# Kernel tuning notes

Measured on AMD Instinct MI355X. Metric: run time of the kernel, lower is better.

## Reference

```python
import jax, jax.numpy as jnp
import numpy as np

B, N, C = 8, 4096, 768
H = 12
D = C // H  # 64


def setup_inputs() -> dict:
    key = jax.random.key(0)
    k1, k2, k3 = jax.random.split(key, 3)
    x = jax.random.normal(k1, (B, N, C), dtype=jnp.float32)
    Wqkv = jax.random.normal(k2, (C, 3 * C), dtype=jnp.float32) * (C ** -0.5)
    Wproj = jax.random.normal(k3, (C, C), dtype=jnp.float32) * (C ** -0.5)
    bproj = jnp.zeros((C,), dtype=jnp.float32)
    return {"x": x, "Wqkv": Wqkv, "Wproj": Wproj, "bproj": bproj}


def reference(x, Wqkv, Wproj, bproj):
    b, n, c = x.shape
    qkv = x @ Wqkv  # [B,N,3C]
    qkv = qkv.reshape(b, n, 3, H, D).transpose(2, 0, 3, 1, 4)  # [3,B,H,N,D]
    q, k, v = qkv[0], qkv[1], qkv[2]
    # softmax over the sequence axis (dim=-2 in torch => N)
    k = jax.nn.softmax(k, axis=-2)
    # context: [B,H,D,D] -- small d x d intermediate
    context = jnp.einsum('bhnd,bhne->bhde', k, v)
    out = jnp.einsum('bhnd,bhde->bhne', q, context)  # [B,H,N,D]
    out = out.transpose(0, 2, 1, 3).reshape(b, n, c)  # b h n d -> b n (h d)
    return out @ Wproj + bproj
```

## Files before the change

kernel.cpp:

```cpp
#include <hip/hip_runtime.h>
#include <cstdint>
#include <cstddef>


typedef __bf16 bf8_t __attribute__((ext_vector_type(8)));
typedef float f4_t __attribute__((ext_vector_type(4)));

#define DEV_INLINE __device__ __forceinline__

DEV_INLINE void gload16(const void* g, void* l) {
  __builtin_amdgcn_global_load_lds(
      (const __attribute__((address_space(1))) void*)g,
      (__attribute__((address_space(3))) void*)l, 16, 0, 0);
}

__global__ __launch_bounds__(256) void cast_f32_bf16(const float* __restrict__ in,
                                                     __bf16* __restrict__ out, int n4) {
  int i = blockIdx.x * 256 + threadIdx.x;
  if (i >= n4) return;
  float4 f = ((const float4*)in)[i];
  union { __bf16 h[4]; uint2 u; } o;
  o.h[0] = (__bf16)f.x; o.h[1] = (__bf16)f.y; o.h[2] = (__bf16)f.z; o.h[3] = (__bf16)f.w;
  ((uint2*)out)[i] = o.u;
}

__global__ __launch_bounds__(256) void transpose_cast(const float* __restrict__ in,
                                                      __bf16* __restrict__ out, int R, int C) {
  __shared__ float t[64][65];
  const int tilesR = R >> 6;
  const int tr = blockIdx.x % tilesR, tc = blockIdx.x / tilesR;
  const int tx = threadIdx.x & 63, ty = threadIdx.x >> 6;
  const int r0 = tr * 64, c0 = tc * 64;
#pragma unroll
  for (int p = 0; p < 16; p++) {
    int r = p * 4 + ty;
    t[r][tx] = in[(size_t)(r0 + r) * C + c0 + tx];
  }
  __syncthreads();
#pragma unroll
  for (int p = 0; p < 16; p++) {
    int c = p * 4 + ty;
    out[(size_t)(c0 + c) * R + r0 + tx] = (__bf16)t[tx][c];
  }
}

__global__ __launch_bounds__(256) void wq_cast(const float* __restrict__ in,
                                               __bf16* __restrict__ out) {
  int o = blockIdx.x * 256 + threadIdx.x;
  int r = o / 768, c = o - r * 768;
  out[o] = (__bf16)in[r * 2304 + c];
}


#define MFMA16(aa, bb, cc) cc = __builtin_amdgcn_mfma_f32_16x16x32_bf16(aa, bb, cc, 0, 0, 0)

#define SAu(buf, u, kc) gload16(gA + (size_t)((u) * 128) * 768 + (kc),        \
                                sA + (buf) * 8192 + (u) * 4096 + tid * 8)
#define SBu(buf, u, kc) gload16(gB + (size_t)((u) * 128) * 768 + (kc),        \
                                sB + (buf) * 8192 + (u) * 4096 + tid * 8)
#define STAGE_T(buf, kc) do { SAu(buf,0,kc); SAu(buf,1,kc); SBu(buf,0,kc); SBu(buf,1,kc); } while (0)

#define G_SETUP()                                                             \
  const int tid = threadIdx.x;                                                \
  const int srow = tid >> 2;                                                  \
  const int gcol = ((tid & 3) ^ (srow & 3)) * 8;                              \
  const int lane = tid & 63, wv = tid >> 6;                                   \
  const int wm = wv >> 2, wn = wv & 3;                                        \
  const int lr = lane & 15, quad = lane >> 4;                                 \
  const int ksw = (quad ^ (lr & 3)) * 8;                                      \
  const int offA0 = (wm * 128 + lr) * 32 + ksw;                               \
  const int offB0 = (wn * 64 + lr) * 32 + ksw;                                \
  f4_t acc[8][4];                                                             \
  _Pragma("unroll") for (int i_ = 0; i_ < 8; i_++)                            \
    _Pragma("unroll") for (int j_ = 0; j_ < 4; j_++)                          \
      acc[i_][j_] = (f4_t){0.f, 0.f, 0.f, 0.f};

#define G_ITER(SA_STAGE, SB_STAGE, TAILV) do {                                \
    const __bf16* aBp = sA + cur * 8192;                                      \
    const __bf16* bBp = sB + cur * 8192;                                      \
    bf8_t a0, a1, a2, a3, b0, b1, b2, b3;                                     \
    a0 = *(const bf8_t*)(aBp + offA0);                                        \
    a1 = *(const bf8_t*)(aBp + offA0 + 512);                                  \
    a2 = *(const bf8_t*)(aBp + offA0 + 1024);                                 \
    a3 = *(const bf8_t*)(aBp + offA0 + 1536);                                 \
    b0 = *(const bf8_t*)(bBp + offB0);                                        \
    b1 = *(const bf8_t*)(bBp + offB0 + 512);                                  \
    b2 = *(const bf8_t*)(bBp + offB0 + 1024);                                 \
    b3 = *(const bf8_t*)(bBp + offB0 + 1536);                                 \
    SA_STAGE;                                                                 \
    __builtin_amdgcn_s_barrier();                                             \
    __builtin_amdgcn_s_setprio(1);                                            \
    MFMA16(a0, b0, acc[0][0]); MFMA16(a0, b1, acc[0][1]);                     \
    MFMA16(a0, b2, acc[0][2]); MFMA16(a0, b3, acc[0][3]);                     \
    MFMA16(a1, b0, acc[1][0]); MFMA16(a1, b1, acc[1][1]);                     \
    MFMA16(a1, b2, acc[1][2]); MFMA16(a1, b3, acc[1][3]);                     \
    MFMA16(a2, b0, acc[2][0]); MFMA16(a2, b1, acc[2][1]);                     \
    MFMA16(a2, b2, acc[2][2]); MFMA16(a2, b3, acc[2][3]);                     \
    MFMA16(a3, b0, acc[3][0]); MFMA16(a3, b1, acc[3][1]);                     \
    MFMA16(a3, b2, acc[3][2]); MFMA16(a3, b3, acc[3][3]);                     \
    __builtin_amdgcn_s_setprio(0);                                            \
    __builtin_amdgcn_s_barrier();                                             \
    a0 = *(const bf8_t*)(aBp + offA0 + 2048);                                 \
    a1 = *(const bf8_t*)(aBp + offA0 + 2560);                                 \
    a2 = *(const bf8_t*)(aBp + offA0 + 3072);                                 \
    a3 = *(const bf8_t*)(aBp + offA0 + 3584);                                 \
    SB_STAGE;                                                                 \
    __builtin_amdgcn_s_barrier();                                             \
    __builtin_amdgcn_s_setprio(1);                                            \
    MFMA16(a0, b0, acc[4][0]); MFMA16(a0, b1, acc[4][1]);                     \
    MFMA16(a0, b2, acc[4][2]); MFMA16(a0, b3, acc[4][3]);                     \
    MFMA16(a1, b0, acc[5][0]); MFMA16(a1, b1, acc[5][1]);                     \
    MFMA16(a1, b2, acc[5][2]); MFMA16(a1, b3, acc[5][3]);                     \
    MFMA16(a2, b0, acc[6][0]); MFMA16(a2, b1, acc[6][1]);                     \
    MFMA16(a2, b2, acc[6][2]); MFMA16(a2, b3, acc[6][3]);                     \
    MFMA16(a3, b0, acc[7][0]); MFMA16(a3, b1, acc[7][1]);                     \
    MFMA16(a3, b2, acc[7][2]); MFMA16(a3, b3, acc[7][3]);                     \
    __builtin_amdgcn_s_setprio(0);                                            \
    TAILV;                                                                    \
    __builtin_amdgcn_s_barrier();                                             \
  } while (0)

#define G_MAIN() do {                                                         \
    STAGE_T(0, 0); STAGE_T(1, 32);                                            \
    asm volatile("s_waitcnt vmcnt(4)" ::: "memory");                          \
    __builtin_amdgcn_s_barrier();                                             \
    int cur = 0;                                                              \
    for (int t = 0; t < 22; t++) {                                            \
      int nx = cur + 2; if (nx > 2) nx -= 3;                                  \
      const int kc = t * 32 + 64;                                             \
      G_ITER({ SAu(nx, 0, kc); SAu(nx, 1, kc); },                             \
             { SBu(nx, 0, kc); SBu(nx, 1, kc); },                             \
             { asm volatile("s_waitcnt vmcnt(4)" ::: "memory"); });           \
      cur++; if (cur > 2) cur = 0;                                            \
    }                                                                         \
    G_ITER({}, {}, { asm volatile("s_waitcnt vmcnt(0)" ::: "memory"); });     \
    cur++; if (cur > 2) cur = 0;                                              \
    G_ITER({}, {}, {});                                                       \
  } while (0)

__global__ __launch_bounds__(512, 2) void gemm1_kv(const __bf16* __restrict__ A,
                                                   const __bf16* __restrict__ B,
                                                   __bf16* __restrict__ KTo,
                                                   __bf16* __restrict__ VTo) {
  __shared__ __bf16 sA[3 * 8192];
  __shared__ __bf16 sB[3 * 8192];
  const int xcd = blockIdx.x & 7, g = blockIdx.x >> 3;
  const int mt = xcd * 16 + g / 6, nt = g % 6;
  G_SETUP();
  const __bf16* gA = A + (size_t)(mt * 256 + srow) * 768 + gcol;
  const __bf16* gB = B + (size_t)(nt * 256 + srow) * 768 + gcol;

  G_MAIN();

  const int sKV = (nt >= 3);
  __bf16* T = sKV ? VTo : KTo;
  const int cw = (nt - sKV * 3) * 256 + wn * 64;
  const int b = mt >> 4;
  const int n0 = (mt & 15) * 256 + wm * 128 + quad * 4;
#pragma unroll
  for (int ci = 0; ci < 4; ci++) {
    int cc = cw + ci * 16;
    __bf16* Tp = T + ((size_t)(b * 12 + (cc >> 6)) * 64 + (cc & 63) + lr) * 4096;
#pragma unroll
    for (int ri = 0; ri < 8; ri++) {
      union { __bf16 h4[4]; uint2 u2; } pk;
#pragma unroll
      for (int r = 0; r < 4; r++) pk.h4[r] = (__bf16)acc[ri][ci][r];
      *(uint2*)&Tp[n0 + ri * 16] = pk.u2;
    }
  }
}

__global__ __launch_bounds__(256) void stats_rows(const __bf16* __restrict__ KT,
                                                  float2* __restrict__ stats) {
  __shared__ float red[8];
  const __bf16* p = KT + (size_t)blockIdx.x * 4096;
  const int tid = threadIdx.x, lane = tid & 63, wv = tid >> 6;
  bf8_t x0 = *(const bf8_t*)&p[tid * 16];
  bf8_t x1 = *(const bf8_t*)&p[tid * 16 + 8];
  float v[16];
#pragma unroll
  for (int k = 0; k < 8; k++) { v[k] = (float)x0[k]; v[8 + k] = (float)x1[k]; }
  float m = v[0];
#pragma unroll
  for (int k = 1; k < 16; k++) m = fmaxf(m, v[k]);
  for (int o = 32; o; o >>= 1) m = fmaxf(m, __shfl_xor(m, o, 64));
  if (lane == 0) red[wv] = m;
  __syncthreads();
  m = fmaxf(fmaxf(red[0], red[1]), fmaxf(red[2], red[3]));
  float s = 0.f;
#pragma unroll
  for (int k = 0; k < 16; k++) s += __expf(v[k] - m);
  for (int o = 32; o; o >>= 1) s += __shfl_xor(s, o, 64);
  if (lane == 0) red[4 + wv] = s;
  __syncthreads();
  if (tid == 0) {
    float st = red[4] + red[5] + red[6] + red[7];
    stats[blockIdx.x] = make_float2(m, 1.0f / st);
  }
}

__global__ __launch_bounds__(256) void ctx_kernel(const __bf16* __restrict__ KT,
                                                  const __bf16* __restrict__ VT,
                                                  const float2* __restrict__ stats,
                                                  float* __restrict__ part) {
  const int bh = blockIdx.x >> 3, kc = blockIdx.x & 7;
  const int tid = threadIdx.x, lane = tid & 63, wv = tid >> 6;
  const int wr = (wv >> 1) * 32, wc = (wv & 1) * 32;
  const int lr = lane & 15, quad = lane >> 4;
  const __bf16* Ab = KT + (size_t)bh * 64 * 4096;
  const __bf16* Bb = VT + (size_t)bh * 64 * 4096;
  float2 st[2];
  st[0] = stats[bh * 64 + wr + lr];
  st[1] = stats[bh * 64 + wr + 16 + lr];
  const f4_t fz = {0.f, 0.f, 0.f, 0.f};
  f4_t acc[2][2] = {{fz, fz}, {fz, fz}};
  const int kbeg = kc * 512;
  for (int k0 = kbeg; k0 < kbeg + 512; k0 += 32) {
    bf8_t a[2], b[2];
#pragma unroll
    for (int i = 0; i < 2; i++) {
      bf8_t raw = *(const bf8_t*)&Ab[(size_t)(wr + i * 16 + lr) * 4096 + k0 + quad * 8];
#pragma unroll
      for (int e = 0; e < 8; e++)
        a[i][e] = (__bf16)(__expf((float)raw[e] - st[i].x) * st[i].y);
    }
#pragma unroll
    for (int j = 0; j < 2; j++)
      b[j] = *(const bf8_t*)&Bb[(size_t)(wc + j * 16 + lr) * 4096 + k0 + quad * 8];
#pragma unroll
    for (int i = 0; i < 2; i++)
#pragma unroll
      for (int j = 0; j < 2; j++)
        acc[i][j] = __builtin_amdgcn_mfma_f32_16x16x32_bf16(a[i], b[j], acc[i][j], 0, 0, 0);
  }
  float* po = part + (size_t)blockIdx.x * 4096;
#pragma unroll
  for (int i = 0; i < 2; i++)
#pragma unroll
    for (int j = 0; j < 2; j++)
#pragma unroll
      for (int r = 0; r < 4; r++)
        po[(wr + i * 16 + quad * 4 + r) * 64 + wc + j * 16 + lr] = acc[i][j][r];
}

__global__ __launch_bounds__(256) void wfused_kernel(const float* __restrict__ part,
                                                     const __bf16* __restrict__ WpT,
                                                     __bf16* __restrict__ B2T) {
  __shared__ __bf16 sctx[64 * 64];
  const int bh = blockIdx.x, cblk = blockIdx.y;
  const int b = bh / 12, h = bh % 12;
  const int tid = threadIdx.x;
  for (int i = tid; i < 4096; i += 256) {
    float s = 0.f;
#pragma unroll
    for (int kc = 0; kc < 8; kc++) s += part[(size_t)(bh * 8 + kc) * 4096 + i];
    sctx[i] = (__bf16)s;
  }
  __syncthreads();
  const int lane = tid & 63, wv = tid >> 6, lr = lane & 15, quad = lane >> 4;
  const int c0 = cblk * 192 + wv * 48;
  const f4_t fz = {0.f, 0.f, 0.f, 0.f};
  f4_t acc[3][4];
#pragma unroll
  for (int i = 0; i < 3; i++)
#pragma unroll
    for (int j = 0; j < 4; j++) acc[i][j] = fz;
#pragma unroll
  for (int k0 = 0; k0 < 64; k0 += 32) {
    bf8_t a[3], bq[4];
#pragma unroll
    for (int i = 0; i < 3; i++)
      a[i] = *(const bf8_t*)&WpT[(size_t)(c0 + i * 16 + lr) * 768 + h * 64 + k0 + quad * 8];
#pragma unroll
    for (int j = 0; j < 4; j++)
      bq[j] = *(const bf8_t*)&sctx[(j * 16 + lr) * 64 + k0 + quad * 8];
#pragma unroll
    for (int i = 0; i < 3; i++)
#pragma unroll
      for (int j = 0; j < 4; j++)
        acc[i][j] = __builtin_amdgcn_mfma_f32_16x16x32_bf16(a[i], bq[j], acc[i][j], 0, 0, 0);
  }
#pragma unroll
  for (int i = 0; i < 3; i++)
#pragma unroll
    for (int j = 0; j < 4; j++)
#pragma unroll
      for (int r = 0; r < 4; r++) {
        int c = c0 + i * 16 + quad * 4 + r;
        int d = j * 16 + lr;
        B2T[((size_t)b * 768 + c) * 768 + h * 64 + d] = (__bf16)acc[i][j][r];
      }
}

__global__ __launch_bounds__(256) void combine_kernel(const __bf16* __restrict__ B2Tall,
                                                      const __bf16* __restrict__ Wq,
                                                      __bf16* __restrict__ Wcomb) {
  constexpr int LD = 768, BK = 32, KTOT = 768;
  __shared__ __bf16 sAc[64 * 32];
  __shared__ __bf16 sBc[64 * 32];
  const int b = blockIdx.x / 144, rem = blockIdx.x % 144;
  const int mt = rem / 12, nt = rem % 12;
  const __bf16* A = B2Tall + (size_t)b * 768 * 768;
  const int tid = threadIdx.x, lane = tid & 63, wv = tid >> 6;
  const int wr = (wv >> 1) * 32, wc = (wv & 1) * 32;
  const int lr = lane & 15, quad = lane >> 4;

  const int e0 = tid * 8;
  const int srow = e0 >> 5, skk = e0 & 31;
  const __bf16* gA = A + (size_t)(mt * 64 + srow) * LD + skk;
  const __bf16* gB = Wq + (size_t)(nt * 64 + srow) * LD + skk;

  const f4_t fz = {0.f, 0.f, 0.f, 0.f};
  f4_t acc[2][2] = {{fz, fz}, {fz, fz}};

  for (int k0 = 0; k0 < KTOT; k0 += BK) {
    gload16(gA, &sAc[e0]);
    gload16(gB, &sBc[e0]);
    gA += BK; gB += BK;
    __syncthreads();
    bf8_t a[2], bq[2];
#pragma unroll
    for (int i = 0; i < 2; i++)
      a[i] = *(const bf8_t*)&sAc[(wr + i * 16 + lr) * 32 + quad * 8];
#pragma unroll
    for (int j = 0; j < 2; j++)
      bq[j] = *(const bf8_t*)&sBc[(wc + j * 16 + lr) * 32 + quad * 8];
#pragma unroll
    for (int i = 0; i < 2; i++)
#pragma unroll
      for (int j = 0; j < 2; j++)
        acc[i][j] = __builtin_amdgcn_mfma_f32_16x16x32_bf16(a[i], bq[j], acc[i][j], 0, 0, 0);
    __syncthreads();
  }
  __bf16* C = Wcomb + (size_t)b * 768 * 768;
  const int row0 = mt * 64 + wr, col0 = nt * 64 + wc;
#pragma unroll
  for (int i = 0; i < 2; i++)
#pragma unroll
    for (int j = 0; j < 2; j++)
#pragma unroll
      for (int r = 0; r < 4; r++)
        C[(size_t)(row0 + i * 16 + quad * 4 + r) * 768 + col0 + j * 16 + lr] =
            (__bf16)acc[i][j][r];
}

__global__ __launch_bounds__(512, 2) void gemm2_out(const __bf16* __restrict__ A,
                                                    const __bf16* __restrict__ Ball,
                                                    float* __restrict__ C,
                                                    const float* __restrict__ bias) {
  __shared__ __bf16 sA[3 * 8192];
  __shared__ __bf16 sB[3 * 8192];
  const int xcd = blockIdx.x & 7, g = blockIdx.x >> 3;
  const int mt = xcd * 16 + g / 3, nt = g % 3;
  const __bf16* B = Ball + (size_t)(mt >> 4) * 768 * 768;
  G_SETUP();
  const __bf16* gA = A + (size_t)(mt * 256 + srow) * 768 + gcol;
  const __bf16* gB = B + (size_t)(nt * 256 + srow) * 768 + gcol;

  G_MAIN();

  const int row0 = mt * 256 + wm * 128 + quad * 4;
  const int col0 = nt * 256 + wn * 64;
#pragma unroll
  for (int ci = 0; ci < 4; ci++) {
    int col = col0 + ci * 16 + lr;
    float bv = bias[col];
#pragma unroll
    for (int ri = 0; ri < 8; ri++) {
#pragma unroll
      for (int r = 0; r < 4; r++)
        C[(size_t)(row0 + ri * 16 + r) * 768 + col] = acc[ri][ci][r] + bv;
    }
  }
}

extern "C" void kernel_launch(void* const* d_in, const int* in_sizes, int n_in,
                              void* d_out, int out_size, void* d_ws, size_t ws_size,
                              hipStream_t stream) {
  const float* x = (const float*)d_in[0];
  const float* Wqkv = (const float*)d_in[1];
  const float* Wproj = (const float*)d_in[2];
  const float* bproj = (const float*)d_in[3];
  float* out = (float*)d_out;

  char* ws = (char*)d_ws;
  __bf16* Xb    = (__bf16*)(ws + 0);
  __bf16* KT    = (__bf16*)(ws + 50331648);
  __bf16* VT    = (__bf16*)(ws + 100663296);
  __bf16* WqkvT = (__bf16*)(ws + 150994944);
  float2* stats = (float2*)(ws + 150994944);
  __bf16* Wqc   = (__bf16*)(ws + 154533888);
  __bf16* WpT   = (__bf16*)(ws + 155713536);
  float*  part  = (float*)(ws + 156893184);
  __bf16* B2T   = (__bf16*)(ws + 169476096);
  __bf16* Wcomb = (__bf16*)(ws + 178913280);

  cast_f32_bf16<<<24576, 256, 0, stream>>>(x, Xb, 25165824 / 4);
  transpose_cast<<<12 * 36, 256, 0, stream>>>(Wqkv, WqkvT, 768, 2304);
  wq_cast<<<(768 * 768) / 256, 256, 0, stream>>>(Wqkv, Wqc);
  transpose_cast<<<12 * 12, 256, 0, stream>>>(Wproj, WpT, 768, 768);
  gemm1_kv<<<768, 512, 0, stream>>>(Xb, WqkvT + 768 * 768, KT, VT);
  stats_rows<<<6144, 256, 0, stream>>>(KT, stats);
  ctx_kernel<<<96 * 8, 256, 0, stream>>>(KT, VT, stats, part);
  wfused_kernel<<<dim3(96, 4), 256, 0, stream>>>(part, WpT, B2T);
  combine_kernel<<<1152, 256, 0, stream>>>(B2T, Wqc, Wcomb);
  gemm2_out<<<384, 512, 0, stream>>>(Xb, Wcomb, out, bproj);
}
```

Measured before the change: 428.5 us.

## Switch shared GEMM mainloop to 32x32x16 MFMA with 64-wide K double buffering

Rewrites the shared GEMM macro used by the KV projection and output projection kernels. It now uses 32x32x16 bf16 MFMA instead of 16x16x32, with K-tiles of 64 and two LDS buffers, replacing K-tiles of 32 with three buffers. The LDS swizzle, the per-lane fragment offsets and both epilogues are remapped to the 32x32 accumulator layout. The goal is fewer LDS reads per MFMA and half as many loop iterations, at the cost of a shallower prefetch pipeline and a full __syncthreads each tile, which can expose global-load latency.

```diff
diff --git a/kernel.cpp b/kernel.cpp
--- a/kernel.cpp
+++ b/kernel.cpp
@@ -5,6 +5,7 @@
 
 typedef __bf16 bf8_t __attribute__((ext_vector_type(8)));
 typedef float f4_t __attribute__((ext_vector_type(4)));
+typedef float f16_t __attribute__((ext_vector_type(16)));
 
 #define DEV_INLINE __device__ __forceinline__
 
@@ -52,121 +53,148 @@
 }
 
 
-#define MFMA16(aa, bb, cc) cc = __builtin_amdgcn_mfma_f32_16x16x32_bf16(aa, bb, cc, 0, 0, 0)
-
-#define SAu(buf, u, kc) gload16(gA + (size_t)((u) * 128) * 768 + (kc),        \
-                                sA + (buf) * 8192 + (u) * 4096 + tid * 8)
-#define SBu(buf, u, kc) gload16(gB + (size_t)((u) * 128) * 768 + (kc),        \
-                                sB + (buf) * 8192 + (u) * 4096 + tid * 8)
-#define STAGE_T(buf, kc) do { SAu(buf,0,kc); SAu(buf,1,kc); SBu(buf,0,kc); SBu(buf,1,kc); } while (0)
+#define MFMA32(aa, bb, cc) cc = __builtin_amdgcn_mfma_f32_32x32x16_bf16(aa, bb, cc, 0, 0, 0)
+
+#define SAu(d, u, kc) gload16(gA + (size_t)((u) * 64) * 768 + (kc),           \
+                              sA + (d) * 16384 + (u) * 4096 + tid * 8)
+#define SBu(d, u, kc) gload16(gB + (size_t)((u) * 64) * 768 + (kc),           \
+                              sB + (d) * 16384 + (u) * 4096 + tid * 8)
 
 #define G_SETUP()                                                             \
   const int tid = threadIdx.x;                                                \
-  const int srow = tid >> 2;                                                  \
-  const int gcol = ((tid & 3) ^ (srow & 3)) * 8;                              \
+  const int gcol = ((tid & 7) ^ ((tid >> 3) & 7)) * 8;                        \
   const int lane = tid & 63, wv = tid >> 6;                                   \
   const int wm = wv >> 2, wn = wv & 3;                                        \
-  const int lr = lane & 15, quad = lane >> 4;                                 \
-  const int ksw = (quad ^ (lr & 3)) * 8;                                      \
-  const int offA0 = (wm * 128 + lr) * 32 + ksw;                               \
-  const int offB0 = (wn * 64 + lr) * 32 + ksw;                                \
-  f4_t acc[8][4];                                                             \
-  _Pragma("unroll") for (int i_ = 0; i_ < 8; i_++)                            \
-    _Pragma("unroll") for (int j_ = 0; j_ < 4; j_++)                          \
-      acc[i_][j_] = (f4_t){0.f, 0.f, 0.f, 0.f};
-
-#define G_ITER(SA_STAGE, SB_STAGE, TAILV) do {                                \
-    const __bf16* aBp = sA + cur * 8192;                                      \
-    const __bf16* bBp = sB + cur * 8192;                                      \
-    bf8_t a0, a1, a2, a3, b0, b1, b2, b3;                                     \
-    a0 = *(const bf8_t*)(aBp + offA0);                                        \
-    a1 = *(const bf8_t*)(aBp + offA0 + 512);                                  \
-    a2 = *(const bf8_t*)(aBp + offA0 + 1024);                                 \
-    a3 = *(const bf8_t*)(aBp + offA0 + 1536);                                 \
-    b0 = *(const bf8_t*)(bBp + offB0);                                        \
-    b1 = *(const bf8_t*)(bBp + offB0 + 512);                                  \
-    b2 = *(const bf8_t*)(bBp + offB0 + 1024);                                 \
-    b3 = *(const bf8_t*)(bBp + offB0 + 1536);                                 \
+  const int l31 = lane & 31, l5 = lane >> 5, key = lane & 7;                  \
+  const int kof0 = ((0 | l5) ^ key) * 8;                                      \
+  const int kof1 = ((2 | l5) ^ key) * 8;                                      \
+  const int kof2 = ((4 | l5) ^ key) * 8;                                      \
+  const int kof3 = ((6 | l5) ^ key) * 8;                                      \
+  const int rowA = (wm * 128 + l31) * 64;                                     \
+  const int rowB = (wn * 64 + l31) * 64;                                      \
+  f16_t acc[4][2];                                                            \
+  _Pragma("unroll") for (int i_ = 0; i_ < 4; i_++)                            \
+    _Pragma("unroll") for (int j_ = 0; j_ < 2; j_++)                          \
+      _Pragma("unroll") for (int e_ = 0; e_ < 16; e_++) acc[i_][j_][e_] = 0.f;
+
+#define G_TILE(SA_STAGE, SB_STAGE) do {                                       \
+    const __bf16* aBp = sA + cur * 16384;                                     \
+    const __bf16* bBp = sB + cur * 16384;                                     \
+    bf8_t a0x, a1x, a2x, a3x, a0y, a1y, a2y, a3y, bq0, bq1;                   \
+                                              \
+    a0x = *(const bf8_t*)(aBp + rowA +        kof0);                          \
+    a1x = *(const bf8_t*)(aBp + rowA + 2048 + kof0);                          \
+    a2x = *(const bf8_t*)(aBp + rowA + 4096 + kof0);                          \
+    a3x = *(const bf8_t*)(aBp + rowA + 6144 + kof0);                          \
+    a0y = *(const bf8_t*)(aBp + rowA +        kof1);                          \
+    a1y = *(const bf8_t*)(aBp + rowA + 2048 + kof1);                          \
+    a2y = *(const bf8_t*)(aBp + rowA + 4096 + kof1);                          \
+    a3y = *(const bf8_t*)(aBp + rowA + 6144 + kof1);                          \
+    bq0 = *(const bf8_t*)(bBp + rowB + kof0);                                 \
+    bq1 = *(const bf8_t*)(bBp + rowB + kof1);                                 \
     SA_STAGE;                                                                 \
     __builtin_amdgcn_s_barrier();                                             \
     __builtin_amdgcn_s_setprio(1);                                            \
-    MFMA16(a0, b0, acc[0][0]); MFMA16(a0, b1, acc[0][1]);                     \
-    MFMA16(a0, b2, acc[0][2]); MFMA16(a0, b3, acc[0][3]);                     \
-    MFMA16(a1, b0, acc[1][0]); MFMA16(a1, b1, acc[1][1]);                     \
-    MFMA16(a1, b2, acc[1][2]); MFMA16(a1, b3, acc[1][3]);                     \
-    MFMA16(a2, b0, acc[2][0]); MFMA16(a2, b1, acc[2][1]);                     \
-    MFMA16(a2, b2, acc[2][2]); MFMA16(a2, b3, acc[2][3]);                     \
-    MFMA16(a3, b0, acc[3][0]); MFMA16(a3, b1, acc[3][1]);                     \
-    MFMA16(a3, b2, acc[3][2]); MFMA16(a3, b3, acc[3][3]);                     \
+    MFMA32(a0x, bq0, acc[0][0]); MFMA32(a0y, bq1, acc[0][0]);                 \
+    MFMA32(a1x, bq0, acc[1][0]); MFMA32(a1y, bq1, acc[1][0]);                 \
+    MFMA32(a2x, bq0, acc[2][0]); MFMA32(a2y, bq1, acc[2][0]);                 \
+    MFMA32(a3x, bq0, acc[3][0]); MFMA32(a3y, bq1, acc[3][0]);                 \
     __builtin_amdgcn_s_setprio(0);                                            \
     __builtin_amdgcn_s_barrier();                                             \
-    a0 = *(const bf8_t*)(aBp + offA0 + 2048);                                 \
-    a1 = *(const bf8_t*)(aBp + offA0 + 2560);                                 \
-    a2 = *(const bf8_t*)(aBp + offA0 + 3072);                                 \
-    a3 = *(const bf8_t*)(aBp + offA0 + 3584);                                 \
+                                                 \
+    bq0 = *(const bf8_t*)(bBp + rowB + 2048 + kof0);                          \
+    bq1 = *(const bf8_t*)(bBp + rowB + 2048 + kof1);                          \
     SB_STAGE;                                                                 \
     __builtin_amdgcn_s_barrier();                                             \
     __builtin_amdgcn_s_setprio(1);                                            \
-    MFMA16(a0, b0, acc[4][0]); MFMA16(a0, b1, acc[4][1]);                     \
-    MFMA16(a0, b2, acc[4][2]); MFMA16(a0, b3, acc[4][3]);                     \
-    MFMA16(a1, b0, acc[5][0]); MFMA16(a1, b1, acc[5][1]);                     \
-    MFMA16(a1, b2, acc[5][2]); MFMA16(a1, b3, acc[5][3]);                     \
-    MFMA16(a2, b0, acc[6][0]); MFMA16(a2, b1, acc[6][1]);                     \
-    MFMA16(a2, b2, acc[6][2]); MFMA16(a2, b3, acc[6][3]);                     \
-    MFMA16(a3, b0, acc[7][0]); MFMA16(a3, b1, acc[7][1]);                     \
-    MFMA16(a3, b2, acc[7][2]); MFMA16(a3, b3, acc[7][3]);                     \
+    MFMA32(a0x, bq0, acc[0][1]); MFMA32(a0y, bq1, acc[0][1]);                 \
+    MFMA32(a1x, bq0, acc[1][1]); MFMA32(a1y, bq1, acc[1][1]);                 \
+    MFMA32(a2x, bq0, acc[2][1]); MFMA32(a2y, bq1, acc[2][1]);                 \
+    MFMA32(a3x, bq0, acc[3][1]); MFMA32(a3y, bq1, acc[3][1]);                 \
     __builtin_amdgcn_s_setprio(0);                                            \
-    TAILV;                                                                    \
-    __builtin_amdgcn_s_barrier();                                             \
+    __builtin_amdgcn_s_barrier();                                             \
+                                              \
+    a0x = *(const bf8_t*)(aBp + rowA +        kof2);                          \
+    a1x = *(const bf8_t*)(aBp + rowA + 2048 + kof2);                          \
+    a2x = *(const bf8_t*)(aBp + rowA + 4096 + kof2);                          \
+    a3x = *(const bf8_t*)(aBp + rowA + 6144 + kof2);                          \
+    a0y = *(const bf8_t*)(aBp + rowA +        kof3);                          \
+    a1y = *(const bf8_t*)(aBp + rowA + 2048 + kof3);                          \
+    a2y = *(const bf8_t*)(aBp + rowA + 4096 + kof3);                          \
+    a3y = *(const bf8_t*)(aBp + rowA + 6144 + kof3);                          \
+    bq0 = *(const bf8_t*)(bBp + rowB + kof2);                                 \
+    bq1 = *(const bf8_t*)(bBp + rowB + kof3);                                 \
+    __builtin_amdgcn_s_barrier();                                             \
+    __builtin_amdgcn_s_setprio(1);                                            \
+    MFMA32(a0x, bq0, acc[0][0]); MFMA32(a0y, bq1, acc[0][0]);                 \
+    MFMA32(a1x, bq0, acc[1][0]); MFMA32(a1y, bq1, acc[1][0]);                 \
+    MFMA32(a2x, bq0, acc[2][0]); MFMA32(a2y, bq1, acc[2][0]);                 \
+    MFMA32(a3x, bq0, acc[3][0]); MFMA32(a3y, bq1, acc[3][0]);                 \
+    __builtin_amdgcn_s_setprio(0);                                            \
+    __builtin_amdgcn_s_barrier();                                             \
+                                                         \
+    bq0 = *(const bf8_t*)(bBp + rowB + 2048 + kof2);                          \
+    bq1 = *(const bf8_t*)(bBp + rowB + 2048 + kof3);                          \
+    __builtin_amdgcn_s_barrier();                                             \
+    __builtin_amdgcn_s_setprio(1);                                            \
+    MFMA32(a0x, bq0, acc[0][1]); MFMA32(a0y, bq1, acc[0][1]);                 \
+    MFMA32(a1x, bq0, acc[1][1]); MFMA32(a1y, bq1, acc[1][1]);                 \
+    MFMA32(a2x, bq0, acc[2][1]); MFMA32(a2y, bq1, acc[2][1]);                 \
+    MFMA32(a3x, bq0, acc[3][1]); MFMA32(a3y, bq1, acc[3][1]);                 \
+    __builtin_amdgcn_s_setprio(0);                                            \
+    __syncthreads();          \
   } while (0)
 
 #define G_MAIN() do {                                                         \
-    STAGE_T(0, 0); STAGE_T(1, 32);                                            \
-    asm volatile("s_waitcnt vmcnt(4)" ::: "memory");                          \
-    __builtin_amdgcn_s_barrier();                                             \
+    SAu(0, 0, 0); SAu(0, 1, 0); SAu(0, 2, 0); SAu(0, 3, 0);                   \
+    SBu(0, 0, 0); SBu(0, 1, 0); SBu(0, 2, 0); SBu(0, 3, 0);                   \
+    __syncthreads();                                                          \
     int cur = 0;                                                              \
-    for (int t = 0; t < 22; t++) {                                            \
-      int nx = cur + 2; if (nx > 2) nx -= 3;                                  \
-      const int kc = t * 32 + 64;                                             \
-      G_ITER({ SAu(nx, 0, kc); SAu(nx, 1, kc); },                             \
-             { SBu(nx, 0, kc); SBu(nx, 1, kc); },                             \
-             { asm volatile("s_waitcnt vmcnt(4)" ::: "memory"); });           \
-      cur++; if (cur > 2) cur = 0;                                            \
+    for (int t = 0; t < 11; ++t) {                                            \
+      const int kcn = (t + 1) * 64;                                           \
+      const int nx = cur ^ 1;                                                 \
+      G_TILE({ SAu(nx, 0, kcn); SAu(nx, 1, kcn);                              \
+               SAu(nx, 2, kcn); SAu(nx, 3, kcn); },                           \
+             { SBu(nx, 0, kcn); SBu(nx, 1, kcn);                              \
+               SBu(nx, 2, kcn); SBu(nx, 3, kcn); });                          \
+      cur = nx;                                                               \
     }                                                                         \
-    G_ITER({}, {}, { asm volatile("s_waitcnt vmcnt(0)" ::: "memory"); });     \
-    cur++; if (cur > 2) cur = 0;                                              \
-    G_ITER({}, {}, {});                                                       \
+    G_TILE({}, {});                                                           \
   } while (0)
 
 __global__ __launch_bounds__(512, 2) void gemm1_kv(const __bf16* __restrict__ A,
                                                    const __bf16* __restrict__ B,
                                                    __bf16* __restrict__ KTo,
                                                    __bf16* __restrict__ VTo) {
-  __shared__ __bf16 sA[3 * 8192];
-  __shared__ __bf16 sB[3 * 8192];
+  __shared__ __bf16 sA[2 * 16384];
+  __shared__ __bf16 sB[2 * 16384];
   const int xcd = blockIdx.x & 7, g = blockIdx.x >> 3;
   const int mt = xcd * 16 + g / 6, nt = g % 6;
   G_SETUP();
-  const __bf16* gA = A + (size_t)(mt * 256 + srow) * 768 + gcol;
-  const __bf16* gB = B + (size_t)(nt * 256 + srow) * 768 + gcol;
+  const __bf16* gA = A + (size_t)(mt * 256 + (tid >> 3)) * 768 + gcol;
+  const __bf16* gB = B + (size_t)(nt * 256 + (tid >> 3)) * 768 + gcol;
 
   G_MAIN();
 
   const int sKV = (nt >= 3);
   __bf16* T = sKV ? VTo : KTo;
-  const int cw = (nt - sKV * 3) * 256 + wn * 64;
-  const int b = mt >> 4;
-  const int n0 = (mt & 15) * 256 + wm * 128 + quad * 4;
-#pragma unroll
-  for (int ci = 0; ci < 4; ci++) {
-    int cc = cw + ci * 16;
-    __bf16* Tp = T + ((size_t)(b * 12 + (cc >> 6)) * 64 + (cc & 63) + lr) * 4096;
-#pragma unroll
-    for (int ri = 0; ri < 8; ri++) {
-      union { __bf16 h4[4]; uint2 u2; } pk;
-#pragma unroll
-      for (int r = 0; r < 4; r++) pk.h4[r] = (__bf16)acc[ri][ci][r];
-      *(uint2*)&Tp[n0 + ri * 16] = pk.u2;
+  const int bb = mt >> 4;
+  const int tok0 = (mt & 15) * 256 + wm * 128 + 4 * l5;
+  const int cbase = (nt - sKV * 3) * 256 + wn * 64;
+#pragma unroll
+  for (int m = 0; m < 4; m++) {
+#pragma unroll
+    for (int n = 0; n < 2; n++) {
+      int c = cbase + n * 32 + l31;
+      __bf16* Tp = T + ((size_t)(bb * 12 + (c >> 6)) * 64 + (c & 63)) * 4096;
+      int tk = tok0 + m * 32;
+#pragma unroll
+      for (int q = 0; q < 4; q++) {
+        union { __bf16 h4[4]; uint2 u2; } pk;
+#pragma unroll
+        for (int r = 0; r < 4; r++) pk.h4[r] = (__bf16)acc[m][n][q * 4 + r];
+        *(uint2*)&Tp[tk + 8 * q] = pk.u2;
+      }
     }
   }
 }
@@ -349,28 +377,32 @@
                                                     const __bf16* __restrict__ Ball,
                                                     float* __restrict__ C,
                                                     const float* __restrict__ bias) {
-  __shared__ __bf16 sA[3 * 8192];
-  __shared__ __bf16 sB[3 * 8192];
+  __shared__ __bf16 sA[2 * 16384];
+  __shared__ __bf16 sB[2 * 16384];
   const int xcd = blockIdx.x & 7, g = blockIdx.x >> 3;
   const int mt = xcd * 16 + g / 3, nt = g % 3;
   const __bf16* B = Ball + (size_t)(mt >> 4) * 768 * 768;
   G_SETUP();
-  const __bf16* gA = A + (size_t)(mt * 256 + srow) * 768 + gcol;
-  const __bf16* gB = B + (size_t)(nt * 256 + srow) * 768 + gcol;
+  const __bf16* gA = A + (size_t)(mt * 256 + (tid >> 3)) * 768 + gcol;
+  const __bf16* gB = B + (size_t)(nt * 256 + (tid >> 3)) * 768 + gcol;
 
   G_MAIN();
 
-  const int row0 = mt * 256 + wm * 128 + quad * 4;
+  const int row0 = mt * 256 + wm * 128 + 4 * l5;
   const int col0 = nt * 256 + wn * 64;
 #pragma unroll
-  for (int ci = 0; ci < 4; ci++) {
-    int col = col0 + ci * 16 + lr;
-    float bv = bias[col];
-#pragma unroll
-    for (int ri = 0; ri < 8; ri++) {
-#pragma unroll
-      for (int r = 0; r < 4; r++)
-        C[(size_t)(row0 + ri * 16 + r) * 768 + col] = acc[ri][ci][r] + bv;
+  for (int m = 0; m < 4; m++) {
+#pragma unroll
+    for (int n = 0; n < 2; n++) {
+      int col = col0 + n * 32 + l31;
+      float bv = bias[col];
+#pragma unroll
+      for (int q = 0; q < 4; q++) {
+        int rb = row0 + m * 32 + 8 * q;
+#pragma unroll
+        for (int r = 0; r < 4; r++)
+          C[(size_t)(rb + r) * 768 + col] = acc[m][n][q * 4 + r] + bv;
+      }
     }
   }
 }
```

After: 411.2 us. 4.1% less time.

## Switch GEMM mainloop to double-buffered 64-wide K tiles with 8-way swizzle

Applied to the files above, without the earlier changes.

Both large GEMMs (gemm1_kv and gemm2_out) now use a K tile of 64 instead of 32. The three-stage ring of 32-wide buffers becomes two 64-wide buffers, and the LDS XOR swizzle widens from 4 to 8 chunks. The A and B loads for the next tile are issued at different points in the four sub-steps, with explicit lgkmcnt waits, so there are fewer outer iterations and barriers per K element. The trade-off is shallower prefetch (two stages), more LDS per block (128KB versus 96KB) and a more intricate buffer-reuse ordering between B loads and reads.

```diff
diff --git a/kernel.cpp b/kernel.cpp
--- a/kernel.cpp
+++ b/kernel.cpp
@@ -54,119 +54,141 @@
 
 #define MFMA16(aa, bb, cc) cc = __builtin_amdgcn_mfma_f32_16x16x32_bf16(aa, bb, cc, 0, 0, 0)
 
-#define SAu(buf, u, kc) gload16(gA + (size_t)((u) * 128) * 768 + (kc),        \
-                                sA + (buf) * 8192 + (u) * 4096 + tid * 8)
-#define SBu(buf, u, kc) gload16(gB + (size_t)((u) * 128) * 768 + (kc),        \
-                                sB + (buf) * 8192 + (u) * 4096 + tid * 8)
-#define STAGE_T(buf, kc) do { SAu(buf,0,kc); SAu(buf,1,kc); SBu(buf,0,kc); SBu(buf,1,kc); } while (0)
+#define SA2(d, h, kc) do {                                                    \
+    gload16(gAt + (size_t)((h) * 128) * 768 + (kc),                           \
+            sA + (d) * 16384 + (h) * 8192 + tid * 8);                         \
+    gload16(gAt + (size_t)((h) * 128 + 64) * 768 + (kc),                      \
+            sA + (d) * 16384 + (h) * 8192 + 4096 + tid * 8);                  \
+  } while (0)
+#define SB2(d, h, kc) do {                                                    \
+    gload16(gBt + (size_t)((h) * 128) * 768 + (kc),                           \
+            sB + (d) * 16384 + (h) * 8192 + tid * 8);                         \
+    gload16(gBt + (size_t)((h) * 128 + 64) * 768 + (kc),                      \
+            sB + (d) * 16384 + (h) * 8192 + 4096 + tid * 8);                  \
+  } while (0)
+#define SA_ALL(d, kc) do { SA2(d, 0, kc); SA2(d, 1, kc); } while (0)
+#define SB_ALL(d, kc) do { SB2(d, 0, kc); SB2(d, 1, kc); } while (0)
 
 #define G_SETUP()                                                             \
   const int tid = threadIdx.x;                                                \
-  const int srow = tid >> 2;                                                  \
-  const int gcol = ((tid & 3) ^ (srow & 3)) * 8;                              \
+  const int srow0 = tid >> 3;                                                 \
+  const int gc0 = ((tid & 7) ^ (srow0 & 7)) * 8;                              \
   const int lane = tid & 63, wv = tid >> 6;                                   \
   const int wm = wv >> 2, wn = wv & 3;                                        \
-  const int lr = lane & 15, quad = lane >> 4;                                 \
-  const int ksw = (quad ^ (lr & 3)) * 8;                                      \
-  const int offA0 = (wm * 128 + lr) * 32 + ksw;                               \
-  const int offB0 = (wn * 64 + lr) * 32 + ksw;                                \
+  const int lr = lane & 15, quad = lane >> 4, key = lr & 7;                   \
+  const int kofs0 = (quad ^ key) * 8;                 \
+  const int kofs1 = ((4 | quad) ^ key) * 8;           \
   f4_t acc[8][4];                                                             \
   _Pragma("unroll") for (int i_ = 0; i_ < 8; i_++)                            \
     _Pragma("unroll") for (int j_ = 0; j_ < 4; j_++)                          \
       acc[i_][j_] = (f4_t){0.f, 0.f, 0.f, 0.f};
 
-#define G_ITER(SA_STAGE, SB_STAGE, TAILV) do {                                \
-    const __bf16* aBp = sA + cur * 8192;                                      \
-    const __bf16* bBp = sB + cur * 8192;                                      \
+#define MROW(ai, mm)                                                          \
+  MFMA16(ai, b0, acc[mm][0]); MFMA16(ai, b1, acc[mm][1]);                     \
+  MFMA16(ai, b2, acc[mm][2]); MFMA16(ai, b3, acc[mm][3]);
+
+#define G_TILE(d, STG1, STG4, TAILV) do {                                     \
+    const __bf16* aB = sA + (d) * 16384 + wm * 8192 + lr * 64;                \
+    const __bf16* bB = sB + (d) * 16384 + (wn >> 1) * 8192 +                  \
+                       (wn & 1) * 4096 + lr * 64;                             \
     bf8_t a0, a1, a2, a3, b0, b1, b2, b3;                                     \
-    a0 = *(const bf8_t*)(aBp + offA0);                                        \
-    a1 = *(const bf8_t*)(aBp + offA0 + 512);                                  \
-    a2 = *(const bf8_t*)(aBp + offA0 + 1024);                                 \
-    a3 = *(const bf8_t*)(aBp + offA0 + 1536);                                 \
-    b0 = *(const bf8_t*)(bBp + offB0);                                        \
-    b1 = *(const bf8_t*)(bBp + offB0 + 512);                                  \
-    b2 = *(const bf8_t*)(bBp + offB0 + 1024);                                 \
-    b3 = *(const bf8_t*)(bBp + offB0 + 1536);                                 \
-    SA_STAGE;                                                                 \
-    __builtin_amdgcn_s_barrier();                                             \
+    a0 = *(const bf8_t*)(aB +        kofs0);                                  \
+    a1 = *(const bf8_t*)(aB + 1024 + kofs0);                                  \
+    a2 = *(const bf8_t*)(aB + 2048 + kofs0);                                  \
+    a3 = *(const bf8_t*)(aB + 3072 + kofs0);                                  \
+    b0 = *(const bf8_t*)(bB +        kofs0);                                  \
+    b1 = *(const bf8_t*)(bB + 1024 + kofs0);                                  \
+    b2 = *(const bf8_t*)(bB + 2048 + kofs0);                                  \
+    b3 = *(const bf8_t*)(bB + 3072 + kofs0);                                  \
+    STG1;                                                                     \
+    __builtin_amdgcn_s_barrier();                                             \
+    asm volatile("s_waitcnt lgkmcnt(0)" ::: "memory");                        \
     __builtin_amdgcn_s_setprio(1);                                            \
-    MFMA16(a0, b0, acc[0][0]); MFMA16(a0, b1, acc[0][1]);                     \
-    MFMA16(a0, b2, acc[0][2]); MFMA16(a0, b3, acc[0][3]);                     \
-    MFMA16(a1, b0, acc[1][0]); MFMA16(a1, b1, acc[1][1]);                     \
-    MFMA16(a1, b2, acc[1][2]); MFMA16(a1, b3, acc[1][3]);                     \
-    MFMA16(a2, b0, acc[2][0]); MFMA16(a2, b1, acc[2][1]);                     \
-    MFMA16(a2, b2, acc[2][2]); MFMA16(a2, b3, acc[2][3]);                     \
-    MFMA16(a3, b0, acc[3][0]); MFMA16(a3, b1, acc[3][1]);                     \
-    MFMA16(a3, b2, acc[3][2]); MFMA16(a3, b3, acc[3][3]);                     \
+    MROW(a0, 0) MROW(a1, 1) MROW(a2, 2) MROW(a3, 3)                           \
     __builtin_amdgcn_s_setprio(0);                                            \
     __builtin_amdgcn_s_barrier();                                             \
-    a0 = *(const bf8_t*)(aBp + offA0 + 2048);                                 \
-    a1 = *(const bf8_t*)(aBp + offA0 + 2560);                                 \
-    a2 = *(const bf8_t*)(aBp + offA0 + 3072);                                 \
-    a3 = *(const bf8_t*)(aBp + offA0 + 3584);                                 \
-    SB_STAGE;                                                                 \
-    __builtin_amdgcn_s_barrier();                                             \
+    a0 = *(const bf8_t*)(aB + 4096 + kofs0);                                  \
+    a1 = *(const bf8_t*)(aB + 5120 + kofs0);                                  \
+    a2 = *(const bf8_t*)(aB + 6144 + kofs0);                                  \
+    a3 = *(const bf8_t*)(aB + 7168 + kofs0);                                  \
+    __builtin_amdgcn_s_barrier();                                             \
+    asm volatile("s_waitcnt lgkmcnt(0)" ::: "memory");                        \
     __builtin_amdgcn_s_setprio(1);                                            \
-    MFMA16(a0, b0, acc[4][0]); MFMA16(a0, b1, acc[4][1]);                     \
-    MFMA16(a0, b2, acc[4][2]); MFMA16(a0, b3, acc[4][3]);                     \
-    MFMA16(a1, b0, acc[5][0]); MFMA16(a1, b1, acc[5][1]);                     \
-    MFMA16(a1, b2, acc[5][2]); MFMA16(a1, b3, acc[5][3]);                     \
-    MFMA16(a2, b0, acc[6][0]); MFMA16(a2, b1, acc[6][1]);                     \
-    MFMA16(a2, b2, acc[6][2]); MFMA16(a2, b3, acc[6][3]);                     \
-    MFMA16(a3, b0, acc[7][0]); MFMA16(a3, b1, acc[7][1]);                     \
-    MFMA16(a3, b2, acc[7][2]); MFMA16(a3, b3, acc[7][3]);                     \
+    MROW(a0, 4) MROW(a1, 5) MROW(a2, 6) MROW(a3, 7)                           \
+    __builtin_amdgcn_s_setprio(0);                                            \
+    __builtin_amdgcn_s_barrier();                                             \
+    a0 = *(const bf8_t*)(aB +        kofs1);                                  \
+    a1 = *(const bf8_t*)(aB + 1024 + kofs1);                                  \
+    a2 = *(const bf8_t*)(aB + 2048 + kofs1);                                  \
+    a3 = *(const bf8_t*)(aB + 3072 + kofs1);                                  \
+    b0 = *(const bf8_t*)(bB +        kofs1);                                  \
+    b1 = *(const bf8_t*)(bB + 1024 + kofs1);                                  \
+    b2 = *(const bf8_t*)(bB + 2048 + kofs1);                                  \
+    b3 = *(const bf8_t*)(bB + 3072 + kofs1);                                  \
+    __builtin_amdgcn_s_barrier();                                             \
+    asm volatile("s_waitcnt lgkmcnt(0)" ::: "memory");                        \
+    __builtin_amdgcn_s_setprio(1);                                            \
+    MROW(a0, 0) MROW(a1, 1) MROW(a2, 2) MROW(a3, 3)                           \
+    __builtin_amdgcn_s_setprio(0);                                            \
+    __builtin_amdgcn_s_barrier();                                             \
+    a0 = *(const bf8_t*)(aB + 4096 + kofs1);                                  \
+    a1 = *(const bf8_t*)(aB + 5120 + kofs1);                                  \
+    a2 = *(const bf8_t*)(aB + 6144 + kofs1);                                  \
+    a3 = *(const bf8_t*)(aB + 7168 + kofs1);                                  \
+    STG4;                                                                     \
+    __builtin_amdgcn_s_barrier();                                             \
+    asm volatile("s_waitcnt lgkmcnt(0)" ::: "memory");                        \
+    __builtin_amdgcn_s_setprio(1);                                            \
+    MROW(a0, 4) MROW(a1, 5) MROW(a2, 6) MROW(a3, 7)                           \
     __builtin_amdgcn_s_setprio(0);                                            \
     TAILV;                                                                    \
     __builtin_amdgcn_s_barrier();                                             \
   } while (0)
 
 #define G_MAIN() do {                                                         \
-    STAGE_T(0, 0); STAGE_T(1, 32);                                            \
+    SA_ALL(0, 0); SB_ALL(0, 0); SB_ALL(1, 64);                                \
     asm volatile("s_waitcnt vmcnt(4)" ::: "memory");                          \
     __builtin_amdgcn_s_barrier();                                             \
-    int cur = 0;                                                              \
-    for (int t = 0; t < 22; t++) {                                            \
-      int nx = cur + 2; if (nx > 2) nx -= 3;                                  \
-      const int kc = t * 32 + 64;                                             \
-      G_ITER({ SAu(nx, 0, kc); SAu(nx, 1, kc); },                             \
-             { SBu(nx, 0, kc); SBu(nx, 1, kc); },                             \
+    for (int t = 0; t < 10; ++t) {                                            \
+      const int d = t & 1;                                                    \
+      const int kA = (t + 1) * 64, kB = (t + 2) * 64;                         \
+      G_TILE(d, { SA_ALL(d ^ 1, kA); }, { SB_ALL(d, kB); },                   \
              { asm volatile("s_waitcnt vmcnt(4)" ::: "memory"); });           \
-      cur++; if (cur > 2) cur = 0;                                            \
     }                                                                         \
-    G_ITER({}, {}, { asm volatile("s_waitcnt vmcnt(0)" ::: "memory"); });     \
-    cur++; if (cur > 2) cur = 0;                                              \
-    G_ITER({}, {}, {});                                                       \
+    G_TILE(0, { SA_ALL(1, 704); }, {},                                        \
+           { asm volatile("s_waitcnt vmcnt(0)" ::: "memory"); });             \
+    G_TILE(1, {}, {}, {});                                                    \
   } while (0)
 
 __global__ __launch_bounds__(512, 2) void gemm1_kv(const __bf16* __restrict__ A,
                                                    const __bf16* __restrict__ B,
                                                    __bf16* __restrict__ KTo,
                                                    __bf16* __restrict__ VTo) {
-  __shared__ __bf16 sA[3 * 8192];
-  __shared__ __bf16 sB[3 * 8192];
+  __shared__ __bf16 sA[2 * 16384];
+  __shared__ __bf16 sB[2 * 16384];
   const int xcd = blockIdx.x & 7, g = blockIdx.x >> 3;
   const int mt = xcd * 16 + g / 6, nt = g % 6;
   G_SETUP();
-  const __bf16* gA = A + (size_t)(mt * 256 + srow) * 768 + gcol;
-  const __bf16* gB = B + (size_t)(nt * 256 + srow) * 768 + gcol;
+  const __bf16* gAt = A + (size_t)(mt * 256 + srow0) * 768 + gc0;
+  const __bf16* gBt = B + (size_t)(nt * 256 + srow0) * 768 + gc0;
 
   G_MAIN();
 
   const int sKV = (nt >= 3);
   __bf16* T = sKV ? VTo : KTo;
-  const int cw = (nt - sKV * 3) * 256 + wn * 64;
-  const int b = mt >> 4;
-  const int n0 = (mt & 15) * 256 + wm * 128 + quad * 4;
-#pragma unroll
-  for (int ci = 0; ci < 4; ci++) {
-    int cc = cw + ci * 16;
-    __bf16* Tp = T + ((size_t)(b * 12 + (cc >> 6)) * 64 + (cc & 63) + lr) * 4096;
-#pragma unroll
-    for (int ri = 0; ri < 8; ri++) {
+  const int bb = mt >> 4;
+  const int tok0 = (mt & 15) * 256 + wm * 128 + quad * 4;
+  const int cbase = (nt - sKV * 3) * 256 + wn * 64;
+#pragma unroll
+  for (int n = 0; n < 4; n++) {
+    int c = cbase + n * 16 + lr;
+    __bf16* Tp = T + ((size_t)(bb * 12 + (c >> 6)) * 64 + (c & 63)) * 4096;
+#pragma unroll
+    for (int m = 0; m < 8; m++) {
       union { __bf16 h4[4]; uint2 u2; } pk;
 #pragma unroll
-      for (int r = 0; r < 4; r++) pk.h4[r] = (__bf16)acc[ri][ci][r];
-      *(uint2*)&Tp[n0 + ri * 16] = pk.u2;
+      for (int r = 0; r < 4; r++) pk.h4[r] = (__bf16)acc[m][n][r];
+      *(uint2*)&Tp[tok0 + m * 16] = pk.u2;
     }
   }
 }
@@ -349,28 +371,28 @@
                                                     const __bf16* __restrict__ Ball,
                                                     float* __restrict__ C,
                                                     const float* __restrict__ bias) {
-  __shared__ __bf16 sA[3 * 8192];
-  __shared__ __bf16 sB[3 * 8192];
+  __shared__ __bf16 sA[2 * 16384];
+  __shared__ __bf16 sB[2 * 16384];
   const int xcd = blockIdx.x & 7, g = blockIdx.x >> 3;
   const int mt = xcd * 16 + g / 3, nt = g % 3;
   const __bf16* B = Ball + (size_t)(mt >> 4) * 768 * 768;
   G_SETUP();
-  const __bf16* gA = A + (size_t)(mt * 256 + srow) * 768 + gcol;
-  const __bf16* gB = B + (size_t)(nt * 256 + srow) * 768 + gcol;
+  const __bf16* gAt = A + (size_t)(mt * 256 + srow0) * 768 + gc0;
+  const __bf16* gBt = B + (size_t)(nt * 256 + srow0) * 768 + gc0;
 
   G_MAIN();
 
   const int row0 = mt * 256 + wm * 128 + quad * 4;
   const int col0 = nt * 256 + wn * 64;
 #pragma unroll
-  for (int ci = 0; ci < 4; ci++) {
-    int col = col0 + ci * 16 + lr;
+  for (int n = 0; n < 4; n++) {
+    int col = col0 + n * 16 + lr;
     float bv = bias[col];
 #pragma unroll
-    for (int ri = 0; ri < 8; ri++) {
+    for (int m = 0; m < 8; m++) {
 #pragma unroll
       for (int r = 0; r < 4; r++)
-        C[(size_t)(row0 + ri * 16 + r) * 768 + col] = acc[ri][ci][r] + bv;
+        C[(size_t)(row0 + m * 16 + r) * 768 + col] = acc[m][n][r] + bv;
     }
   }
 }
```

Measured after the change: 425.2 us. Within noise of the previous version (-0.8%).
